# Performance work log

Hardware: AMD Instinct MI355X
Metric: run time of the kernel (lower is better)

## Reference

```python
import jax, jax.numpy as jnp
import numpy as np
from jax import lax

NPOINT = 1024
K = 32
EPS = 1e-5  # BatchNorm eps (eval mode, running stats)


def _fps(xyz, npoint):
    """Farthest point sampling. xyz: [B,N,3] -> idx [B,npoint] (int32).
    Deterministic start at index 0 (torch version starts at a random index)."""
    B, N, _ = xyz.shape
    barange = jnp.arange(B)

    def step(carry, _):
        distance, farthest = carry
        centroid = xyz[barange, farthest]                    # [B,3]
        d = jnp.sum((xyz - centroid[:, None, :]) ** 2, -1)   # [B,N]
        distance = jnp.minimum(distance, d)
        new_far = jnp.argmax(distance, axis=-1).astype(jnp.int32)
        return (distance, new_far), farthest

    init = (jnp.full((B, N), 1e10, dtype=xyz.dtype), jnp.zeros((B,), jnp.int32))
    _, centroids = lax.scan(step, init, None, length=npoint)  # [npoint,B]
    return centroids.T                                        # [B,npoint]


def _square_distance(src, dst):
    # src [B,M,3], dst [B,N,3] -> [B,M,N]
    return (jnp.sum(src ** 2, -1)[:, :, None]
            - 2.0 * jnp.einsum('bmc,bnc->bmn', src, dst)
            + jnp.sum(dst ** 2, -1)[:, None, :])


def _gather(p, idx):
    # p [B,N,C], idx [B,...] -> [B,...,C]
    return jax.vmap(lambda pb, ib: pb[ib])(p, idx)


def _mlp_layer(x, w, cb, g, b, m, v):
    # x [B,S,K,Cin]; Conv2d 1x1 == channel matmul, then eval-mode BN, ReLU
    x = jnp.einsum('bskc,oc->bsko', x, w) + cb
    x = (x - m) * (g / jnp.sqrt(v + EPS)) + b
    return jax.nn.relu(x)


def _forward(xyz, points, w0, cb0, g0, b0, m0, v0,
             w1, cb1, g1, b1, m1, v1, w2, cb2, g2, b2, m2, v2):
    fps_idx = _fps(xyz, NPOINT)                       # [B,S]
    new_xyz = _gather(xyz, fps_idx)                   # [B,S,3]
    dists = _square_distance(new_xyz, xyz)            # [B,S,N]
    _, nn_idx = lax.top_k(-dists, K)                  # [B,S,K]
    grouped_xyz = _gather(xyz, nn_idx)                # [B,S,K,3]
    grouped_xyz_norm = grouped_xyz - new_xyz[:, :, None, :]
    grouped_pts = _gather(points, nn_idx)             # [B,S,K,C]
    x = jnp.concatenate([grouped_xyz_norm, grouped_pts], axis=-1)  # [B,S,K,3+C]
    x = _mlp_layer(x, w0, cb0, g0, b0, m0, v0)
    x = _mlp_layer(x, w1, cb1, g1, b1, m1, v1)
    x = _mlp_layer(x, w2, cb2, g2, b2, m2, v2)
    new_points = jnp.max(x, axis=2)                   # max over K -> [B,S,Cout]
    return new_xyz, jnp.transpose(new_points, (0, 2, 1))  # [B,Cout,S]


def setup_inputs() -> dict:
    key = jax.random.key(0)
    ks = jax.random.split(key, 8)
    B, N, C = 16, 4096, 64
    inp = {
        'xyz': jax.random.normal(ks[0], (B, N, 3), jnp.float32),
        'points': jax.random.normal(ks[1], (B, N, C), jnp.float32),
    }
    channels = [(3 + C, 64), (64, 64), (64, 128)]
    for li, (ci, co) in enumerate(channels):
        inp[f'w{li}'] = jax.random.normal(ks[2 + li], (co, ci), jnp.float32) * 0.05
        inp[f'cb{li}'] = jnp.zeros((co,), jnp.float32)
        inp[f'g{li}'] = jnp.ones((co,), jnp.float32)
        inp[f'b{li}'] = jnp.zeros((co,), jnp.float32)
        inp[f'm{li}'] = jnp.zeros((co,), jnp.float32)
        inp[f'v{li}'] = jnp.ones((co,), jnp.float32)
    return inp


def reference(xyz, points, w0, cb0, g0, b0, m0, v0,
              w1, cb1, g1, b1, m1, v1, w2, cb2, g2, b2, m2, v2):
    return _forward(xyz, points, w0, cb0, g0, b0, m0, v0,
                    w1, cb1, g1, b1, m1, v1, w2, cb2, g2, b2, m2, v2)
```

## Files before the change

kernel.cpp:

```cpp
#include <hip/hip_runtime.h>
#include <math.h>

#define NPTS 4096
#define NB 16
#define NS 1024
#define KNB 32
#define CPTS 64

#define FLAG_OFF_B  0
#define CNT_OFF_B   64
#define PUBC_OFF_B  128
#define WFRAG_ELEMS 18432
#define NUNITS      16384
#define CAP         256
#define GRAB        8

typedef __attribute__((ext_vector_type(8))) short short8;
typedef __attribute__((ext_vector_type(4))) float f32x4;

__device__ __forceinline__ short f2bf(float f) {
  unsigned u = __float_as_uint(f);
  unsigned r = (u + 0x7fffu + ((u >> 16) & 1u)) >> 16;
  return (short)r;
}

template <int CTRL>
__device__ __forceinline__ int dppmov(int cur) {
  return __builtin_amdgcn_update_dpp(cur, cur, CTRL, 0xF, 0xF, false);
}
template <int CTRL>
__device__ __forceinline__ void dpp_max_u64(unsigned& hi, unsigned& lo) {
  unsigned nhi = (unsigned)dppmov<CTRL>((int)hi);
  unsigned nlo = (unsigned)dppmov<CTRL>((int)lo);
  bool gt = (nhi > hi) || (nhi == hi && nlo > lo);
  hi = gt ? nhi : hi;
  lo = gt ? nlo : lo;
}
template <int CTRL>
__device__ __forceinline__ void dpp_fmax(float& m) {
  m = fmaxf(m, __int_as_float(dppmov<CTRL>(__float_as_int(m))));
}
template <int CTRL>
__device__ __forceinline__ void dpp_umin(unsigned& v) {
  unsigned o = (unsigned)dppmov<CTRL>((int)v);
  v = (o < v) ? o : v;
}

#define XSTR 104
__global__ __launch_bounds__(512, 2) void fused_kernel(
    const float* __restrict__ xyz, const float* __restrict__ points,
    const float* __restrict__ w0, const float* __restrict__ cb0, const float* __restrict__ g0,
    const float* __restrict__ b0, const float* __restrict__ m0, const float* __restrict__ v0,
    const float* __restrict__ w1, const float* __restrict__ cb1, const float* __restrict__ g1,
    const float* __restrict__ b1, const float* __restrict__ m1, const float* __restrict__ v1,
    const float* __restrict__ w2, const float* __restrict__ cb2, const float* __restrict__ g2,
    const float* __restrict__ b2, const float* __restrict__ m2, const float* __restrict__ v2,
    char* __restrict__ wsb, float* __restrict__ newxyz, float* __restrict__ outp) {
  struct FpsSh {
    float4 sxyz4[NPTS];
    float4 centL[NS];
    unsigned long long part[2][8];
  };
  struct WorkerSh {
    short Wlds[WFRAG_ELEMS];
    short X[8][32 * XSTR];
    unsigned long long cand[8][CAP];
    int nnL[8][KNB];
    float biasL[256];
    unsigned cnt[8];
  };
  __shared__ union { FpsSh f; WorkerSh w; } sh;

  const int t = threadIdx.x;
  const int lane = t & 63;
  const int wave = t >> 6;
  unsigned* flagp = (unsigned*)(wsb + FLAG_OFF_B);
  unsigned* cntp  = (unsigned*)(wsb + CNT_OFF_B);
  float* pubC = (float*)(wsb + PUBC_OFF_B);

  if (blockIdx.x < NB) {
    const int b = blockIdx.x;
    const float* xb = xyz + (size_t)b * NPTS * 3;
    float* outb = newxyz + (size_t)b * NS * 3;

    for (int i = t; i < NPTS; i += 512)
      sh.f.sxyz4[i] = make_float4(xb[i * 3 + 0], xb[i * 3 + 1], xb[i * 3 + 2], 0.f);

    float px[8], py[8], pz[8], dist[8];
#pragma unroll
    for (int j = 0; j < 8; ++j) {
      int n = t + 512 * j;
      px[j] = xb[n * 3 + 0];
      py[j] = xb[n * 3 + 1];
      pz[j] = xb[n * 3 + 2];
      dist[j] = 1e10f;
    }
    __syncthreads();
    float cx = sh.f.sxyz4[0].x, cy = sh.f.sxyz4[0].y, cz = sh.f.sxyz4[0].z;
    if (t == 0) sh.f.centL[0] = sh.f.sxyz4[0];

    for (int it = 1; it < NS; ++it) {
      const int buf = it & 1;
      float dm[8];
#pragma unroll
      for (int j = 0; j < 8; ++j) {
        float dx = __fsub_rn(px[j], cx);
        float dy = __fsub_rn(py[j], cy);
        float dz = __fsub_rn(pz[j], cz);
        float d  = __fadd_rn(__fadd_rn(__fmul_rn(dx, dx), __fmul_rn(dy, dy)), __fmul_rn(dz, dz));
        float v  = fminf(dist[j], d);
        dist[j] = v;
        dm[j] = v;
      }
      float m = fmaxf(fmaxf(fmaxf(dm[0], dm[1]), fmaxf(dm[2], dm[3])),
                      fmaxf(fmaxf(dm[4], dm[5]), fmaxf(dm[6], dm[7])));
      dpp_fmax<0xB1>(m);  dpp_fmax<0x4E>(m);  dpp_fmax<0x141>(m);
      dpp_fmax<0x140>(m); dpp_fmax<0x142>(m); dpp_fmax<0x143>(m);
      float M = __int_as_float(__builtin_amdgcn_readlane(__float_as_int(m), 63));
      unsigned i0 = (dm[0] == M) ? (unsigned)(t + 512 * 0) : 0xFFFFFFFFu;
      unsigned i1 = (dm[1] == M) ? (unsigned)(t + 512 * 1) : 0xFFFFFFFFu;
      unsigned i2 = (dm[2] == M) ? (unsigned)(t + 512 * 2) : 0xFFFFFFFFu;
      unsigned i3 = (dm[3] == M) ? (unsigned)(t + 512 * 3) : 0xFFFFFFFFu;
      unsigned i4 = (dm[4] == M) ? (unsigned)(t + 512 * 4) : 0xFFFFFFFFu;
      unsigned i5 = (dm[5] == M) ? (unsigned)(t + 512 * 5) : 0xFFFFFFFFu;
      unsigned i6 = (dm[6] == M) ? (unsigned)(t + 512 * 6) : 0xFFFFFFFFu;
      unsigned i7 = (dm[7] == M) ? (unsigned)(t + 512 * 7) : 0xFFFFFFFFu;
      unsigned a01 = i0 < i1 ? i0 : i1, a23 = i2 < i3 ? i2 : i3;
      unsigned a45 = i4 < i5 ? i4 : i5, a67 = i6 < i7 ? i6 : i7;
      unsigned a03 = a01 < a23 ? a01 : a23, a47 = a45 < a67 ? a45 : a67;
      unsigned idxl = a03 < a47 ? a03 : a47;
      dpp_umin<0xB1>(idxl);  dpp_umin<0x4E>(idxl);  dpp_umin<0x141>(idxl);
      dpp_umin<0x140>(idxl); dpp_umin<0x142>(idxl); dpp_umin<0x143>(idxl);
      if (lane == 63)
        sh.f.part[buf][wave] = ((unsigned long long)__float_as_uint(M) << 32) | (unsigned)(~idxl);
      __syncthreads();
      unsigned long long k0 = sh.f.part[buf][lane & 7];
      unsigned khi = (unsigned)(k0 >> 32), klo = (unsigned)k0;
      dpp_max_u64<0xB1>(khi, klo);
      dpp_max_u64<0x4E>(khi, klo);
      dpp_max_u64<0x141>(khi, klo);
      int bi = (int)(~klo) & 4095;
      float4 c4 = sh.f.sxyz4[bi];
      cx = c4.x; cy = c4.y; cz = c4.z;
      if (t == 0) sh.f.centL[it] = c4;
      if ((it & 31) == 31 && wave == 0) {
        if (lane == 0) {
          asm volatile("s_waitcnt vmcnt(0)" ::: "memory");
          __hip_atomic_store(&flagp[b], (unsigned)(it - 31), __ATOMIC_RELAXED, __HIP_MEMORY_SCOPE_AGENT);
        }
        if (lane < 32) {
          int ci = it - 31 + lane;
          float4 cc = sh.f.centL[ci];
          float* dst = pubC + ((size_t)b * NS + ci) * 3;
          __hip_atomic_store(dst + 0, cc.x, __ATOMIC_RELAXED, __HIP_MEMORY_SCOPE_AGENT);
          __hip_atomic_store(dst + 1, cc.y, __ATOMIC_RELAXED, __HIP_MEMORY_SCOPE_AGENT);
          __hip_atomic_store(dst + 2, cc.z, __ATOMIC_RELAXED, __HIP_MEMORY_SCOPE_AGENT);
        }
      }
    }
    if (wave == 0 && lane == 0) {
      asm volatile("s_waitcnt vmcnt(0)" ::: "memory");
      __hip_atomic_store(&flagp[b], (unsigned)NS, __ATOMIC_RELAXED, __HIP_MEMORY_SCOPE_AGENT);
    }
    __syncthreads();
    const float* cf = (const float*)sh.f.centL;
    for (int i = t; i < NS * 3; i += 512) {
      int p = i / 3, c = i - p * 3;
      outb[i] = cf[p * 4 + c];
    }
  }

  __syncthreads();
  for (int i = t; i < WFRAG_ELEMS; i += 512) {
    int g = i >> 9, ln = (i >> 3) & 63, j = i & 7;
    int l, nt, s;
    if (g < 12)      { l = 0; nt = g / 3;  s = g % 3; }
    else if (g < 20) { l = 1; int gg = g - 12; nt = gg >> 1; s = gg & 1; }
    else             { l = 2; int gg = g - 20; nt = gg >> 1; s = gg & 1; }
    int n = nt * 16 + (ln & 15);
    int k = s * 32 + ((ln >> 4) << 3) + j;
    float val = 0.f;
    if (l == 0) {
      float sc = g0[n] / sqrtf(v0[n] + 1e-5f);
      if (k < 64)      val = w0[n * 67 + (k + 3)] * sc;
      else if (k < 67) val = w0[n * 67 + (k - 64)] * sc;
    }
    else if (l == 1) { val = w1[n * 64 + k] * (g1[n] / sqrtf(v1[n] + 1e-5f)); }
    else { val = w2[n * 64 + k] * (g2[n] / sqrtf(v2[n] + 1e-5f)); }
    sh.w.Wlds[i] = f2bf(val);
  }
  if (t < 256) {
    int o = t;
    float bv;
    if (o < 64)       { float sc = g0[o] / sqrtf(v0[o] + 1e-5f); bv = (cb0[o] - m0[o]) * sc + b0[o]; }
    else if (o < 128) { int c = o - 64;  float sc = g1[c] / sqrtf(v1[c] + 1e-5f); bv = (cb1[c] - m1[c]) * sc + b1[c]; }
    else              { int c = o - 128; float sc = g2[c] / sqrtf(v2[c] + 1e-5f); bv = (cb2[c] - m2[c]) * sc + b2[c]; }
    sh.w.biasL[o] = bv;
  }
  __syncthreads();

  unsigned long long* cand = sh.w.cand[wave];
  for (int i = lane; i < (32 * XSTR) / 2; i += 64) ((int*)sh.w.X[wave])[i] = 0;

  unsigned fcache = 0;

  for (;;) {
    unsigned base = 0;
    if (lane == 0) base = atomicAdd(cntp, (unsigned)GRAB);
    base = (unsigned)__builtin_amdgcn_readfirstlane((int)base);
    if (base >= NUNITS) break;
    unsigned uend = base + GRAB;
    if (uend > NUNITS) uend = NUNITS;

    for (unsigned u = base; u < uend; ++u) {
    const int b = (int)(u & 15u);
    const int s = (int)(u >> 4);

    {
      unsigned need = (unsigned)s + 1u;
      unsigned have = (unsigned)__shfl((int)fcache, b, 64);
      if (have < need) {
        unsigned f;
        for (;;) {
          f = __hip_atomic_load(&flagp[b], __ATOMIC_RELAXED, __HIP_MEMORY_SCOPE_AGENT);
          if (f >= need) break;
          __builtin_amdgcn_s_sleep(64);
        }
        if (lane == b) fcache = f;
        asm volatile("" ::: "memory");
      }
    }
    const float* qcp = pubC + ((size_t)b * NS + s) * 3;
    float qx = __hip_atomic_load(qcp + 0, __ATOMIC_RELAXED, __HIP_MEMORY_SCOPE_AGENT);
    float qy = __hip_atomic_load(qcp + 1, __ATOMIC_RELAXED, __HIP_MEMORY_SCOPE_AGENT);
    float qz = __hip_atomic_load(qcp + 2, __ATOMIC_RELAXED, __HIP_MEMORY_SCOPE_AGENT);

    const float* xb = xyz + (size_t)b * NPTS * 3;
    float s2 = __fadd_rn(__fadd_rn(__fmul_rn(qx, qx), __fmul_rn(qy, qy)), __fmul_rn(qz, qz));

    unsigned long long mkey = 0xFFFFFFFFFFFFFFFFull;
#pragma unroll 4
    for (int j = 0; j < 64; ++j) {
      int n = j * 64 + lane;
      float px = xb[n * 3], py = xb[n * 3 + 1], pz = xb[n * 3 + 2];
      float n2 = __fadd_rn(__fadd_rn(__fmul_rn(px, px), __fmul_rn(py, py)), __fmul_rn(pz, pz));
      float dt = __fadd_rn(__fadd_rn(__fmul_rn(qx, px), __fmul_rn(qy, py)), __fmul_rn(qz, pz));
      float d  = __fadd_rn(__fsub_rn(s2, __fmul_rn(2.0f, dt)), n2);
      unsigned uu = __float_as_uint(d);
      uu ^= (0x80000000u | (unsigned)((int)uu >> 31));
      unsigned long long key = ((unsigned long long)uu << 32) | (unsigned)n;
      mkey = key < mkey ? key : mkey;
    }

    {
      unsigned mh = (unsigned)(mkey >> 32), ml2 = (unsigned)mkey;
#pragma unroll
      for (int k = 2; k <= 64; k <<= 1) {
#pragma unroll
        for (int j = k >> 1; j >= 1; j >>= 1) {
          unsigned oh = (unsigned)__shfl_xor((int)mh, j, 64);
          unsigned ol = (unsigned)__shfl_xor((int)ml2, j, 64);
          bool up = (lane & k) == 0;
          bool lower = (lane & j) == 0;
          bool omin = (oh < mh) || (oh == mh && ol < ml2);
          bool keep_o = (lower == up) ? omin : !omin;
          mh = keep_o ? oh : mh;
          ml2 = keep_o ? ol : ml2;
        }
      }
      unsigned th = (unsigned)__builtin_amdgcn_readlane((int)mh, 31);
      unsigned tl = (unsigned)__builtin_amdgcn_readlane((int)ml2, 31);
      mkey = ((unsigned long long)th << 32) | tl;
    }
    const unsigned long long tau = mkey;

    if (lane == 0) sh.w.cnt[wave] = 0;
    asm volatile("s_waitcnt lgkmcnt(0)" ::: "memory");
#pragma unroll 4
    for (int j = 0; j < 64; ++j) {
      int n = j * 64 + lane;
      float px = xb[n * 3], py = xb[n * 3 + 1], pz = xb[n * 3 + 2];
      float n2 = __fadd_rn(__fadd_rn(__fmul_rn(px, px), __fmul_rn(py, py)), __fmul_rn(pz, pz));
      float dt = __fadd_rn(__fadd_rn(__fmul_rn(qx, px), __fmul_rn(qy, py)), __fmul_rn(qz, pz));
      float d  = __fadd_rn(__fsub_rn(s2, __fmul_rn(2.0f, dt)), n2);
      unsigned uu = __float_as_uint(d);
      uu ^= (0x80000000u | (unsigned)((int)uu >> 31));
      unsigned long long key = ((unsigned long long)uu << 32) | (unsigned)n;
      if (key <= tau) {
        unsigned pos = atomicAdd(&sh.w.cnt[wave], 1u);
        if (pos < CAP) cand[pos] = key;
      }
    }
    asm volatile("s_waitcnt lgkmcnt(0)" ::: "memory");
    unsigned cn = sh.w.cnt[wave];
    if (cn > CAP) cn = CAP;

    for (unsigned bb = 0; bb < cn; bb += 64) {
      unsigned i = bb + (unsigned)lane;
      unsigned long long ki = (i < cn) ? cand[i] : 0xFFFFFFFFFFFFFFFFull;
      int rank = 0;
#pragma unroll 4
      for (unsigned c2 = 0; c2 < cn; ++c2)
        rank += (cand[c2] < ki) ? 1 : 0;
      if (i < cn && rank < KNB) sh.w.nnL[wave][rank] = (int)(unsigned)(ki & 0xFFFFFFFFull);
    }
    asm volatile("s_waitcnt lgkmcnt(0)" ::: "memory");

    {
      const int qi = wave;
      const float* pb = points + (size_t)b * NPTS * CPTS;
      const float* bias = sh.w.biasL;
      short* X = sh.w.X[qi];

      {
        int h = lane & 1, r = lane >> 1;
        int idx = sh.w.nnL[qi][r];
        const f32x4* src = (const f32x4*)(pb + (size_t)idx * CPTS) + h * 8;
        short8* dst = (short8*)&X[r * XSTR + h * 32];
#pragma unroll
        for (int q = 0; q < 4; ++q) {
          f32x4 v0 = src[q * 2], v1 = src[q * 2 + 1];
          short8 o;
          o[0] = f2bf(v0[0]); o[1] = f2bf(v0[1]); o[2] = f2bf(v0[2]); o[3] = f2bf(v0[3]);
          o[4] = f2bf(v1[0]); o[5] = f2bf(v1[1]); o[6] = f2bf(v1[2]); o[7] = f2bf(v1[3]);
          dst[q] = o;
        }
      }
      if (lane < 32) {
        int idx = sh.w.nnL[qi][lane];
        X[lane * XSTR + 64] = f2bf(__fsub_rn(xb[idx * 3 + 0], qx));
        X[lane * XSTR + 65] = f2bf(__fsub_rn(xb[idx * 3 + 1], qy));
        X[lane * XSTR + 66] = f2bf(__fsub_rn(xb[idx * 3 + 2], qz));
      }

      const int ml = lane & 15, quad = lane >> 4;
      const short8* Wf = (const short8*)sh.w.Wlds;

      short8 a0[2][3];
#pragma unroll
      for (int m2 = 0; m2 < 2; ++m2)
#pragma unroll
        for (int s3 = 0; s3 < 3; ++s3)
          a0[m2][s3] = *(const short8*)&X[(m2 * 16 + ml) * XSTR + s3 * 32 + quad * 8];
      f32x4 acc0[2][4];
#pragma unroll
      for (int m2 = 0; m2 < 2; ++m2)
#pragma unroll
        for (int nt = 0; nt < 4; ++nt) {
          f32x4 c = {0.f, 0.f, 0.f, 0.f};
#pragma unroll
          for (int s3 = 0; s3 < 3; ++s3)
            c = __builtin_amdgcn_mfma_f32_16x16x32_bf16(a0[m2][s3], Wf[(nt * 3 + s3) * 64 + lane], c, 0, 0, 0);
          acc0[m2][nt] = c;
        }
#pragma unroll
      for (int m2 = 0; m2 < 2; ++m2)
#pragma unroll
        for (int nt = 0; nt < 4; ++nt) {
          int ch = nt * 16 + ml;
          float bv = bias[ch];
#pragma unroll
          for (int r4 = 0; r4 < 4; ++r4) {
            float y = fmaxf(acc0[m2][nt][r4] + bv, 0.f);
            int m = quad * 4 + r4;
            int sK = ch >> 5, qq = (ch >> 3) & 3, jj = ch & 7;
            X[((m2 * 2 + sK) * 64 + qq * 16 + m) * 8 + jj] = f2bf(y);
          }
        }

      short8 a1[2][2];
#pragma unroll
      for (int m2 = 0; m2 < 2; ++m2)
#pragma unroll
        for (int sK = 0; sK < 2; ++sK)
          a1[m2][sK] = *(const short8*)&X[((m2 * 2 + sK) * 64 + lane) * 8];
      f32x4 acc1[2][4];
#pragma unroll
      for (int m2 = 0; m2 < 2; ++m2)
#pragma unroll
        for (int nt = 0; nt < 4; ++nt) {
          f32x4 c = {0.f, 0.f, 0.f, 0.f};
#pragma unroll
          for (int sK = 0; sK < 2; ++sK)
            c = __builtin_amdgcn_mfma_f32_16x16x32_bf16(a1[m2][sK], Wf[(12 + nt * 2 + sK) * 64 + lane], c, 0, 0, 0);
          acc1[m2][nt] = c;
        }
#pragma unroll
      for (int m2 = 0; m2 < 2; ++m2)
#pragma unroll
        for (int nt = 0; nt < 4; ++nt) {
          int ch = nt * 16 + ml;
          float bv = bias[64 + ch];
#pragma unroll
          for (int r4 = 0; r4 < 4; ++r4) {
            float y = fmaxf(acc1[m2][nt][r4] + bv, 0.f);
            int m = quad * 4 + r4;
            int sK = ch >> 5, qq = (ch >> 3) & 3, jj = ch & 7;
            X[((m2 * 2 + sK) * 64 + qq * 16 + m) * 8 + jj] = f2bf(y);
          }
        }

      short8 a2[2][2];
#pragma unroll
      for (int m2 = 0; m2 < 2; ++m2)
#pragma unroll
        for (int sK = 0; sK < 2; ++sK)
          a2[m2][sK] = *(const short8*)&X[((m2 * 2 + sK) * 64 + lane) * 8];
#pragma unroll
      for (int nt = 0; nt < 8; ++nt) {
        f32x4 c0 = {0.f, 0.f, 0.f, 0.f}, c1 = {0.f, 0.f, 0.f, 0.f};
        short8 w0f = Wf[(20 + nt * 2 + 0) * 64 + lane];
        short8 w1f = Wf[(20 + nt * 2 + 1) * 64 + lane];
        c0 = __builtin_amdgcn_mfma_f32_16x16x32_bf16(a2[0][0], w0f, c0, 0, 0, 0);
        c0 = __builtin_amdgcn_mfma_f32_16x16x32_bf16(a2[0][1], w1f, c0, 0, 0, 0);
        c1 = __builtin_amdgcn_mfma_f32_16x16x32_bf16(a2[1][0], w0f, c1, 0, 0, 0);
        c1 = __builtin_amdgcn_mfma_f32_16x16x32_bf16(a2[1][1], w1f, c1, 0, 0, 0);
        float bv = bias[128 + nt * 16 + ml];
        float m = -1.f;
#pragma unroll
        for (int r4 = 0; r4 < 4; ++r4) {
          m = fmaxf(m, fmaxf(c0[r4] + bv, 0.f));
          m = fmaxf(m, fmaxf(c1[r4] + bv, 0.f));
        }
        m = fmaxf(m, __shfl_xor(m, 16, 64));
        m = fmaxf(m, __shfl_xor(m, 32, 64));
        if (lane < 16) outp[((size_t)b * 128 + nt * 16 + lane) * NS + s] = m;
      }
    }
    }
  }
}

extern "C" void kernel_launch(void* const* d_in, const int* in_sizes, int n_in,
                              void* d_out, int out_size, void* d_ws, size_t ws_size,
                              hipStream_t stream) {
  const float* xyz    = (const float*)d_in[0];
  const float* points = (const float*)d_in[1];
  const float* w0  = (const float*)d_in[2];
  const float* cb0 = (const float*)d_in[3];
  const float* g0  = (const float*)d_in[4];
  const float* b0  = (const float*)d_in[5];
  const float* m0  = (const float*)d_in[6];
  const float* v0  = (const float*)d_in[7];
  const float* w1  = (const float*)d_in[8];
  const float* cb1 = (const float*)d_in[9];
  const float* g1  = (const float*)d_in[10];
  const float* b1  = (const float*)d_in[11];
  const float* m1  = (const float*)d_in[12];
  const float* v1  = (const float*)d_in[13];
  const float* w2  = (const float*)d_in[14];
  const float* cb2 = (const float*)d_in[15];
  const float* g2  = (const float*)d_in[16];
  const float* b2  = (const float*)d_in[17];
  const float* m2  = (const float*)d_in[18];
  const float* v2  = (const float*)d_in[19];

  char*  wsb    = (char*)d_ws;
  float* newxyz = (float*)d_out;
  float* outp   = (float*)d_out + (size_t)NB * NS * 3;

  hipMemsetAsync(wsb, 0, 128, stream);
  fused_kernel<<<256, 512, 0, stream>>>(
      xyz, points, w0, cb0, g0, b0, m0, v0, w1, cb1, g1, b1, m1, v1,
      w2, cb2, g2, b2, m2, v2, wsb, newxyz, outp);
}
```

Baseline: 1.028 ms.

## Pack FPS distance and index into f64 key and use packed-f32 math

Rewrites the farthest-point-sampling inner loop so each point's min-distance and inverted index are packed into one double. A single f64 max reduction across lanes and waves then replaces the separate float max, equality check and index-min passes. Distance math uses two-wide float vectors so the compiler can emit packed FP32 ops, with fp contraction disabled to keep rounding unchanged. The worker grab size also drops from 8 to 2. The f64 compare is valid only because the distances are non-negative, and the f64 max rate may limit the gain.

```diff
diff --git a/kernel.cpp b/kernel.cpp
--- a/kernel.cpp
+++ b/kernel.cpp
@@ -1,5 +1,7 @@
 #include <hip/hip_runtime.h>
 #include <math.h>
+
+#pragma clang fp contract(off)
 
 #define NPTS 4096
 #define NB 16
@@ -13,10 +15,11 @@
 #define WFRAG_ELEMS 18432
 #define NUNITS      16384
 #define CAP         256
-#define GRAB        8
+#define GRAB        2
 
 typedef __attribute__((ext_vector_type(8))) short short8;
 typedef __attribute__((ext_vector_type(4))) float f32x4;
+typedef __attribute__((ext_vector_type(2))) float f32x2;
 
 __device__ __forceinline__ short f2bf(float f) {
   unsigned u = __float_as_uint(f);
@@ -29,21 +32,13 @@
   return __builtin_amdgcn_update_dpp(cur, cur, CTRL, 0xF, 0xF, false);
 }
 template <int CTRL>
-__device__ __forceinline__ void dpp_max_u64(unsigned& hi, unsigned& lo) {
-  unsigned nhi = (unsigned)dppmov<CTRL>((int)hi);
-  unsigned nlo = (unsigned)dppmov<CTRL>((int)lo);
-  bool gt = (nhi > hi) || (nhi == hi && nlo > lo);
-  hi = gt ? nhi : hi;
-  lo = gt ? nlo : lo;
-}
-template <int CTRL>
-__device__ __forceinline__ void dpp_fmax(float& m) {
-  m = fmaxf(m, __int_as_float(dppmov<CTRL>(__float_as_int(m))));
-}
-template <int CTRL>
-__device__ __forceinline__ void dpp_umin(unsigned& v) {
-  unsigned o = (unsigned)dppmov<CTRL>((int)v);
-  v = (o < v) ? o : v;
+__device__ __forceinline__ double dpp_fmax64(double x) {
+  int hi = __double2hiint(x), lo = __double2loint(x);
+  double o = __hiloint2double(dppmov<CTRL>(hi), dppmov<CTRL>(lo));
+  return fmax(x, o);
+}
+__device__ __forceinline__ double mkkey(float d, unsigned lo) {
+  return __hiloint2double((int)__float_as_uint(d), (int)lo);
 }
 
 #define XSTR 104
@@ -86,14 +81,17 @@
     for (int i = t; i < NPTS; i += 512)
       sh.f.sxyz4[i] = make_float4(xb[i * 3 + 0], xb[i * 3 + 1], xb[i * 3 + 2], 0.f);
 
-    float px[8], py[8], pz[8], dist[8];
-#pragma unroll
-    for (int j = 0; j < 8; ++j) {
-      int n = t + 512 * j;
-      px[j] = xb[n * 3 + 0];
-      py[j] = xb[n * 3 + 1];
-      pz[j] = xb[n * 3 + 2];
-      dist[j] = 1e10f;
+    f32x2 px2[4], py2[4], pz2[4], d2[4];
+    unsigned lo8[8];
+#pragma unroll
+    for (int j = 0; j < 8; ++j) lo8[j] = ~(unsigned)(t + 512 * j);
+#pragma unroll
+    for (int j2 = 0; j2 < 4; ++j2) {
+      int n0 = t + 512 * (2 * j2), n1 = t + 512 * (2 * j2 + 1);
+      px2[j2].x = xb[n0 * 3 + 0]; px2[j2].y = xb[n1 * 3 + 0];
+      py2[j2].x = xb[n0 * 3 + 1]; py2[j2].y = xb[n1 * 3 + 1];
+      pz2[j2].x = xb[n0 * 3 + 2]; pz2[j2].y = xb[n1 * 3 + 2];
+      d2[j2].x = 1e10f; d2[j2].y = 1e10f;
     }
     __syncthreads();
     float cx = sh.f.sxyz4[0].x, cy = sh.f.sxyz4[0].y, cz = sh.f.sxyz4[0].z;
@@ -101,45 +99,33 @@
 
     for (int it = 1; it < NS; ++it) {
       const int buf = it & 1;
-      float dm[8];
-#pragma unroll
-      for (int j = 0; j < 8; ++j) {
-        float dx = __fsub_rn(px[j], cx);
-        float dy = __fsub_rn(py[j], cy);
-        float dz = __fsub_rn(pz[j], cz);
-        float d  = __fadd_rn(__fadd_rn(__fmul_rn(dx, dx), __fmul_rn(dy, dy)), __fmul_rn(dz, dz));
-        float v  = fminf(dist[j], d);
-        dist[j] = v;
-        dm[j] = v;
-      }
-      float m = fmaxf(fmaxf(fmaxf(dm[0], dm[1]), fmaxf(dm[2], dm[3])),
-                      fmaxf(fmaxf(dm[4], dm[5]), fmaxf(dm[6], dm[7])));
-      dpp_fmax<0xB1>(m);  dpp_fmax<0x4E>(m);  dpp_fmax<0x141>(m);
-      dpp_fmax<0x140>(m); dpp_fmax<0x142>(m); dpp_fmax<0x143>(m);
-      float M = __int_as_float(__builtin_amdgcn_readlane(__float_as_int(m), 63));
-      unsigned i0 = (dm[0] == M) ? (unsigned)(t + 512 * 0) : 0xFFFFFFFFu;
-      unsigned i1 = (dm[1] == M) ? (unsigned)(t + 512 * 1) : 0xFFFFFFFFu;
-      unsigned i2 = (dm[2] == M) ? (unsigned)(t + 512 * 2) : 0xFFFFFFFFu;
-      unsigned i3 = (dm[3] == M) ? (unsigned)(t + 512 * 3) : 0xFFFFFFFFu;
-      unsigned i4 = (dm[4] == M) ? (unsigned)(t + 512 * 4) : 0xFFFFFFFFu;
-      unsigned i5 = (dm[5] == M) ? (unsigned)(t + 512 * 5) : 0xFFFFFFFFu;
-      unsigned i6 = (dm[6] == M) ? (unsigned)(t + 512 * 6) : 0xFFFFFFFFu;
-      unsigned i7 = (dm[7] == M) ? (unsigned)(t + 512 * 7) : 0xFFFFFFFFu;
-      unsigned a01 = i0 < i1 ? i0 : i1, a23 = i2 < i3 ? i2 : i3;
-      unsigned a45 = i4 < i5 ? i4 : i5, a67 = i6 < i7 ? i6 : i7;
-      unsigned a03 = a01 < a23 ? a01 : a23, a47 = a45 < a67 ? a45 : a67;
-      unsigned idxl = a03 < a47 ? a03 : a47;
-      dpp_umin<0xB1>(idxl);  dpp_umin<0x4E>(idxl);  dpp_umin<0x141>(idxl);
-      dpp_umin<0x140>(idxl); dpp_umin<0x142>(idxl); dpp_umin<0x143>(idxl);
+      f32x2 cax; cax.x = cx; cax.y = cx;
+      f32x2 cay; cay.x = cy; cay.y = cy;
+      f32x2 caz; caz.x = cz; caz.y = cz;
+      double kk[8];
+#pragma unroll
+      for (int j2 = 0; j2 < 4; ++j2) {
+        f32x2 dx = px2[j2] - cax;
+        f32x2 dy = py2[j2] - cay;
+        f32x2 dz = pz2[j2] - caz;
+        f32x2 dd = (dx * dx + dy * dy) + dz * dz;
+        f32x2 dv = d2[j2];
+        dv.x = fminf(dv.x, dd.x);
+        dv.y = fminf(dv.y, dd.y);
+        d2[j2] = dv;
+        kk[2 * j2]     = mkkey(dv.x, lo8[2 * j2]);
+        kk[2 * j2 + 1] = mkkey(dv.y, lo8[2 * j2 + 1]);
+      }
+      double km = fmax(fmax(fmax(kk[0], kk[1]), fmax(kk[2], kk[3])),
+                       fmax(fmax(kk[4], kk[5]), fmax(kk[6], kk[7])));
+      km = dpp_fmax64<0xB1>(km);  km = dpp_fmax64<0x4E>(km);  km = dpp_fmax64<0x141>(km);
+      km = dpp_fmax64<0x140>(km); km = dpp_fmax64<0x142>(km); km = dpp_fmax64<0x143>(km);
       if (lane == 63)
-        sh.f.part[buf][wave] = ((unsigned long long)__float_as_uint(M) << 32) | (unsigned)(~idxl);
+        sh.f.part[buf][wave] = (unsigned long long)__double_as_longlong(km);
       __syncthreads();
-      unsigned long long k0 = sh.f.part[buf][lane & 7];
-      unsigned khi = (unsigned)(k0 >> 32), klo = (unsigned)k0;
-      dpp_max_u64<0xB1>(khi, klo);
-      dpp_max_u64<0x4E>(khi, klo);
-      dpp_max_u64<0x141>(khi, klo);
-      int bi = (int)(~klo) & 4095;
+      double kw = __longlong_as_double((long long)sh.f.part[buf][lane & 7]);
+      kw = dpp_fmax64<0xB1>(kw); kw = dpp_fmax64<0x4E>(kw); kw = dpp_fmax64<0x141>(kw);
+      int bi = (int)(~(unsigned)__double2loint(kw)) & 4095;
       float4 c4 = sh.f.sxyz4[bi];
       cx = c4.x; cy = c4.y; cz = c4.z;
       if (t == 0) sh.f.centL[it] = c4;
```

Result: faster. 880.3 us (-14.4%).
